# Performance work log

Hardware: AMD Instinct MI355X
Metric: run time of the kernel (lower is better)

The kernel has to match this reference:

```python
import jax, jax.numpy as jnp
import numpy as np

B, P, V, L = 256, 512, 8, 16
N = B * P            # 131072 nodes
C = V * L            # 128 in_channels (== out_channels, forced by the .view in forward)
H = 4                # heads
DOUT = 128           # out_channels per head
E = N * 5            # k=5 neighbors per node
NEG_SLOPE = 0.2


def setup_inputs() -> dict:
    key = jax.random.key(0)
    ks = jax.random.split(key, 8)
    patches = jax.random.normal(ks[0], (B, P, V, L), dtype=jnp.float32)
    edge_index = jax.random.randint(ks[1], (2, E), 0, N, dtype=jnp.int64)
    s = 1.0 / np.sqrt(C)
    W_gat = jax.random.uniform(ks[2], (C, H * DOUT), dtype=jnp.float32, minval=-s, maxval=s)
    att_src = jax.random.uniform(ks[3], (H, DOUT), dtype=jnp.float32, minval=-s, maxval=s)
    att_dst = jax.random.uniform(ks[4], (H, DOUT), dtype=jnp.float32, minval=-s, maxval=s)
    bias_gat = jnp.zeros((H * DOUT,), dtype=jnp.float32)
    s2 = 1.0 / np.sqrt(H * DOUT)
    W_lin = jax.random.uniform(ks[5], (H * DOUT, DOUT), dtype=jnp.float32, minval=-s2, maxval=s2)
    b_lin = jax.random.uniform(ks[6], (DOUT,), dtype=jnp.float32, minval=-s2, maxval=s2)
    return {"patches": patches, "edge_index": edge_index, "W_gat": W_gat,
            "att_src": att_src, "att_dst": att_dst, "bias_gat": bias_gat,
            "W_lin": W_lin, "b_lin": b_lin}


def reference(patches, edge_index, W_gat, att_src, att_dst, bias_gat, W_lin, b_lin):
    b, p, v, l = patches.shape
    n = b * p
    x = patches.reshape(n, v * l)                      # [N, C]
    xw = (x @ W_gat).reshape(n, H, DOUT)               # [N, H, D]
    # PyG GATConv default add_self_loops=True
    loops = jnp.arange(n, dtype=edge_index.dtype)
    src = jnp.concatenate([edge_index[0], loops])      # message source j
    dst = jnp.concatenate([edge_index[1], loops])      # message target i
    a_src = jnp.einsum('nhd,hd->nh', xw, att_src)      # [N, H]
    a_dst = jnp.einsum('nhd,hd->nh', xw, att_dst)
    e = jax.nn.leaky_relu(a_src[src] + a_dst[dst], NEG_SLOPE)   # [Etot, H]
    m = jax.ops.segment_max(e, dst, num_segments=n)
    ex = jnp.exp(e - m[dst])
    denom = jax.ops.segment_sum(ex, dst, num_segments=n)
    alpha = ex / (denom[dst] + 1e-16)                  # segment softmax over in-edges
    out = jax.ops.segment_sum(alpha[:, :, None] * xw[src], dst, num_segments=n)  # [N, H, D]
    out = out.reshape(n, H * DOUT) + bias_gat
    out = jax.nn.elu(out)
    out = out @ W_lin + b_lin                          # [N, DOUT]
    return out.reshape(b, p, v, l)
```

## Files before the change

kernel.cpp:

```cpp
#include <hip/hip_runtime.h>
#include <hip/hip_bf16.h>
#include <stdint.h>

#define N_NODES 131072
#define C_IN    128
#define HEADS   4
#define DHEAD   128
#define HD      512
#define E_EDGES 655360
#define NEG_SLOPE 0.2f
#define NCHUNK  4
#define CHUNK_N (N_NODES / NCHUNK)
#define SCAN_B  (N_NODES / 256)

typedef short bf16x8 __attribute__((ext_vector_type(8)));
typedef float f32x4  __attribute__((ext_vector_type(4)));

__device__ __forceinline__ float bf2f(unsigned short u) {
    unsigned int x = ((unsigned int)u) << 16;
    return __builtin_bit_cast(float, x);
}
__device__ __forceinline__ unsigned short f2bf(float f) {
    unsigned int u = __builtin_bit_cast(unsigned int, f);
    unsigned int r = u + 0x7FFFu + ((u >> 16) & 1u);
    return (unsigned short)(r >> 16);
}
__device__ __forceinline__ float lrelu(float v) {
    return v > 0.0f ? v : NEG_SLOPE * v;
}

__global__ void detect_kernel(const unsigned int* p_f, const unsigned int* p_i, int* flags) {
    int lane = threadIdx.x;
    int cnt = 0;
#pragma unroll
    for (int r = 0; r < 4; r++) {
        unsigned int e = (p_f[lane + 64 * r] >> 7) & 0xFFu;
        cnt += (e >= 110u && e <= 137u) ? 1 : 0;
    }
    int z = 0;
#pragma unroll
    for (int r = 0; r < 2; r++) {
        z += (p_i[2 * (lane + 64 * r) + 1] == 0u) ? 1 : 0;
    }
#pragma unroll
    for (int o = 1; o < 64; o <<= 1) {
        cnt += __shfl_xor(cnt, o, 64);
        z   += __shfl_xor(z, o, 64);
    }
    if (lane == 0) {
        flags[0] = (cnt >= 128) ? 1 : 0;
        flags[1] = (z == 128) ? 1 : 0;
    }
}

__global__ void conv_w1(const void* in, unsigned short* out, const int* flags) {
    int idx = blockIdx.x * blockDim.x + threadIdx.x;
    int n = idx >> 7, k = idx & 127;
    float v = flags[0] ? bf2f(((const unsigned short*)in)[k * HD + n])
                       : ((const float*)in)[k * HD + n];
    out[idx] = f2bf(v);
}

__global__ void conv_w2(const void* in, unsigned short* out, const int* flags) {
    int idx = blockIdx.x * blockDim.x + threadIdx.x;
    int n = idx >> 9, k = idx & 511;
    float v = flags[0] ? bf2f(((const unsigned short*)in)[k * DHEAD + n])
                       : ((const float*)in)[k * DHEAD + n];
    out[idx] = f2bf(v);
}

__global__ void conv_small(const void* as, const void* ad, const void* bg, const void* bl,
                           float* att_s, float* att_d, float* bias_g, float* b_lin,
                           const int* flags) {
    int i = blockIdx.x * blockDim.x + threadIdx.x;
    bool bf = flags[0] != 0;
    if (i < 512) {
        att_s[i] = bf ? bf2f(((const unsigned short*)as)[i]) : ((const float*)as)[i];
    } else if (i < 1024) {
        int j = i - 512;
        att_d[j] = bf ? bf2f(((const unsigned short*)ad)[j]) : ((const float*)ad)[j];
    } else if (i < 1536) {
        int j = i - 1024;
        bias_g[j] = bf ? bf2f(((const unsigned short*)bg)[j]) : ((const float*)bg)[j];
    } else if (i < 1664) {
        int j = i - 1536;
        b_lin[j] = bf ? bf2f(((const unsigned short*)bl)[j]) : ((const float*)bl)[j];
    }
}

__global__ void conv_edges_hist(const void* in, int* src32, int* dst32, int* deg,
                                const int* flags) {
    int i = blockIdx.x * blockDim.x + threadIdx.x;
    if (i >= 2 * E_EDGES) return;
    int v = flags[1] ? (int)((const long long*)in)[i] : ((const int*)in)[i];
    if (i < E_EDGES) {
        src32[i] = v;
    } else {
        dst32[i - E_EDGES] = v;
        atomicAdd(&deg[v], 1);
    }
}

__global__ void zero_deg(int* deg) {
    int i = blockIdx.x * blockDim.x + threadIdx.x;
    deg[i] = 0;
}

__global__ void scan_local(const int* __restrict__ deg, int* __restrict__ offv,
                           int* __restrict__ bsums) {
    __shared__ int tmp[256];
    int t = threadIdx.x;
    int g = blockIdx.x * 256 + t;
    int v = deg[g];
    tmp[t] = v;
    __syncthreads();
#pragma unroll
    for (int d = 1; d < 256; d <<= 1) {
        int x = (t >= d) ? tmp[t - d] : 0;
        __syncthreads();
        tmp[t] += x;
        __syncthreads();
    }
    offv[g] = tmp[t] - v;
    if (t == 255) bsums[blockIdx.x] = tmp[t];
}

__global__ void scan_bsums(int* bsums) {
    __shared__ int tmp[SCAN_B];
    int t = threadIdx.x;
    int v = bsums[t];
    tmp[t] = v;
    __syncthreads();
#pragma unroll
    for (int d = 1; d < SCAN_B; d <<= 1) {
        int x = (t >= d) ? tmp[t - d] : 0;
        __syncthreads();
        tmp[t] += x;
        __syncthreads();
    }
    bsums[t] = tmp[t] - v;
}

__global__ void scan_apply(int* __restrict__ offv, const int* __restrict__ bsums,
                           int* __restrict__ cursor) {
    int g = blockIdx.x * 256 + threadIdx.x;
    int v = offv[g] + bsums[blockIdx.x];
    offv[g] = v;
    cursor[g] = v;
}

__global__ void scatter_kernel(const int* src32, const int* dst32, int* cursor, int* csr) {
    int i = blockIdx.x * blockDim.x + threadIdx.x;
    int d = dst32[i];
    int pos = atomicAdd(&cursor[d], 1);
    csr[pos] = src32[i];
}

__launch_bounds__(256)
__global__ void gemm1_fused(const void* __restrict__ Ain,
                            const unsigned short* __restrict__ BT,
                            const float* __restrict__ attS, const float* __restrict__ attD,
                            unsigned short* __restrict__ xw,
                            float* __restrict__ aSrc, float* __restrict__ aDst,
                            const int* __restrict__ flags) {
    __shared__ unsigned short lA[128 * 136];
    __shared__ unsigned short lB[128 * 136];
    __shared__ float dS[2][128];
    __shared__ float dD[2][128];
    int tid = threadIdx.x;
    int m0 = blockIdx.x * 128;

    if (flags[0] == 0) {
        const float* Af = (const float*)Ain;
#pragma unroll
        for (int p = 0; p < 16; p++) {
            int l = p * 256 + tid;
            int r = l >> 5, c = (l & 31) * 4;
            float4 f = *(const float4*)&Af[(size_t)(m0 + r) * C_IN + c];
            unsigned short t4[4] = {f2bf(f.x), f2bf(f.y), f2bf(f.z), f2bf(f.w)};
            *(uint2*)&lA[r * 136 + c] = *(const uint2*)t4;
        }
    } else {
        const unsigned short* Ab = (const unsigned short*)Ain;
#pragma unroll
        for (int p = 0; p < 8; p++) {
            int l = p * 256 + tid;
            int r = l >> 4, c = (l & 15) * 8;
            *(uint4*)&lA[r * 136 + c] = *(const uint4*)&Ab[(size_t)(m0 + r) * C_IN + c];
        }
    }

    int wid = tid >> 6, lane = tid & 63;
    int wr = (wid >> 1) * 64, wc = (wid & 1) * 64;
    int lr = lane & 15, half = lane >> 4;
    int slot = wid & 1;

    for (int ct = 0; ct < HEADS; ct++) {
#pragma unroll
        for (int p = 0; p < 8; p++) {
            int l = p * 256 + tid;
            int r = l >> 4, c = (l & 15) * 8;
            *(uint4*)&lB[r * 136 + c] = *(const uint4*)&BT[(size_t)(ct * 128 + r) * C_IN + c];
        }
        __syncthreads();

        f32x4 acc[4][4];
#pragma unroll
        for (int i = 0; i < 4; i++)
#pragma unroll
            for (int j = 0; j < 4; j++) acc[i][j] = (f32x4){0.f, 0.f, 0.f, 0.f};

#pragma unroll
        for (int kk = 0; kk < 4; kk++) {
            bf16x8 af[4], bfr[4];
#pragma unroll
            for (int i = 0; i < 4; i++)
                af[i] = *(const bf16x8*)&lA[(wr + i * 16 + lr) * 136 + kk * 32 + half * 8];
#pragma unroll
            for (int j = 0; j < 4; j++)
                bfr[j] = *(const bf16x8*)&lB[(wc + j * 16 + lr) * 136 + kk * 32 + half * 8];
#pragma unroll
            for (int i = 0; i < 4; i++)
#pragma unroll
                for (int j = 0; j < 4; j++)
                    acc[i][j] = __builtin_amdgcn_mfma_f32_16x16x32_bf16(af[i], bfr[j], acc[i][j], 0, 0, 0);
        }

        const float* aS = attS + ct * DHEAD;
        const float* aD = attD + ct * DHEAD;
#pragma unroll
        for (int i = 0; i < 4; i++) {
#pragma unroll
            for (int r = 0; r < 4; r++) {
                float ps = 0.f, pd = 0.f;
#pragma unroll
                for (int j = 0; j < 4; j++) {
                    float v = acc[i][j][r];
                    int col = wc + j * 16 + lr;
                    ps += v * aS[col];
                    pd += v * aD[col];
                }
#pragma unroll
                for (int o = 1; o < 16; o <<= 1) {
                    ps += __shfl_xor(ps, o, 64);
                    pd += __shfl_xor(pd, o, 64);
                }
                if (lr == 0) {
                    int row = wr + i * 16 + half * 4 + r;
                    dS[slot][row] = ps;
                    dD[slot][row] = pd;
                }
            }
        }
        __syncthreads();

#pragma unroll
        for (int i = 0; i < 4; i++)
#pragma unroll
            for (int j = 0; j < 4; j++)
#pragma unroll
                for (int r = 0; r < 4; r++)
                    lB[(wr + i * 16 + half * 4 + r) * 136 + wc + j * 16 + lr] = f2bf(acc[i][j][r]);
        __syncthreads();

#pragma unroll
        for (int p = 0; p < 8; p++) {
            int l = p * 256 + tid;
            int r = l >> 4, c = (l & 15) * 8;
            *(uint4*)&xw[(size_t)(m0 + r) * HD + ct * 128 + c] = *(const uint4*)&lB[r * 136 + c];
        }
        if (tid < 128) {
            aSrc[(size_t)(m0 + tid) * HEADS + ct] = dS[0][tid] + dS[1][tid];
        } else {
            int t = tid - 128;
            aDst[(size_t)(m0 + t) * HEADS + ct] = dD[0][t] + dD[1][t];
        }
        __syncthreads();
    }
}

__launch_bounds__(256)
__global__ void gemm2(const unsigned short* __restrict__ A,
                      const unsigned short* __restrict__ BT,
                      const float* __restrict__ bias,
                      unsigned short* Cbf, float* Cf,
                      const int* __restrict__ flags, long long rowOff) {
    __shared__ unsigned short smem[64 * 136];
    unsigned short* lA = smem;
    unsigned short* lB = smem + 64 * 40;
    int tid = threadIdx.x;
    int m0 = blockIdx.x * 64;
    int wid = tid >> 6, lane = tid & 63;
    int wr = (wid >> 1) * 32, wc = (wid & 1) * 64;
    int lr = lane & 15, half = lane >> 4;

    f32x4 acc[2][4];
#pragma unroll
    for (int i = 0; i < 2; i++)
#pragma unroll
        for (int j = 0; j < 4; j++) acc[i][j] = (f32x4){0.f, 0.f, 0.f, 0.f};

    for (int k0 = 0; k0 < HD; k0 += 32) {
        {
            int r = tid >> 2, c = (tid & 3) * 8;
            *(uint4*)&lA[r * 40 + c] = *(const uint4*)&A[(size_t)(m0 + r) * HD + k0 + c];
        }
#pragma unroll
        for (int p = 0; p < 2; p++) {
            int l = p * 256 + tid;
            int r = l >> 2, c = (l & 3) * 8;
            *(uint4*)&lB[r * 40 + c] = *(const uint4*)&BT[(size_t)r * HD + k0 + c];
        }
        __syncthreads();
        bf16x8 af[2], bfr[4];
#pragma unroll
        for (int i = 0; i < 2; i++)
            af[i] = *(const bf16x8*)&lA[(wr + i * 16 + lr) * 40 + half * 8];
#pragma unroll
        for (int j = 0; j < 4; j++)
            bfr[j] = *(const bf16x8*)&lB[(wc + j * 16 + lr) * 40 + half * 8];
#pragma unroll
        for (int i = 0; i < 2; i++)
#pragma unroll
            for (int j = 0; j < 4; j++)
                acc[i][j] = __builtin_amdgcn_mfma_f32_16x16x32_bf16(af[i], bfr[j], acc[i][j], 0, 0, 0);
        __syncthreads();
    }

    if (flags[0] != 0) {
#pragma unroll
        for (int i = 0; i < 2; i++)
#pragma unroll
            for (int j = 0; j < 4; j++) {
                int gcol = wc + j * 16 + lr;
                float b = bias[gcol];
#pragma unroll
                for (int r = 0; r < 4; r++)
                    smem[(wr + i * 16 + half * 4 + r) * 136 + gcol] = f2bf(acc[i][j][r] + b);
            }
        __syncthreads();
#pragma unroll
        for (int p = 0; p < 2; p++) {
            int l = p * 256 + tid;
            int r = l >> 4, c = (l & 15) * 8;
            *(uint4*)&Cbf[(size_t)(rowOff + m0 + r) * DHEAD + c] = *(const uint4*)&smem[r * 136 + c];
        }
    } else {
#pragma unroll
        for (int i = 0; i < 2; i++)
#pragma unroll
            for (int j = 0; j < 4; j++) {
                int gcol = wc + j * 16 + lr;
                float b = bias[gcol];
#pragma unroll
                for (int r = 0; r < 4; r++) {
                    int grow = m0 + wr + i * 16 + half * 4 + r;
                    Cf[(size_t)(rowOff + grow) * DHEAD + gcol] = acc[i][j][r] + b;
                }
            }
    }
}

__launch_bounds__(256)
__global__ void aggregate(const unsigned short* __restrict__ xw,
                          const float* __restrict__ a_src, const float* __restrict__ a_dst,
                          const int* __restrict__ off, const int* __restrict__ deg,
                          const int* __restrict__ csr, const float* __restrict__ bias_g,
                          unsigned short* __restrict__ y, int nodeBase) {
    int local = blockIdx.x * 4 + (threadIdx.x >> 6);
    int node = nodeBase + local;
    int l = threadIdx.x & 63;
    int h = l >> 4;
    int ebase = l * 8;
    int o = off[node], dn = deg[node];
    float ad = a_dst[node * HEADS + h];

    float acc[8];
    float denom;
    {
        float w = __expf(lrelu(a_src[node * HEADS + h] + ad));
        uint4 q = *(const uint4*)&xw[(size_t)node * HD + ebase];
        const unsigned short* u = (const unsigned short*)&q;
        denom = w;
#pragma unroll
        for (int k = 0; k < 8; k++) acc[k] = w * bf2f(u[k]);
    }

    for (int e0 = 0; e0 < dn; e0 += 8) {
        int   idx[8];
        float as[8];
        uint4 px[8];
#pragma unroll
        for (int b = 0; b < 8; b++)
            idx[b] = (e0 + b < dn) ? csr[o + e0 + b] : node;
#pragma unroll
        for (int b = 0; b < 8; b++)
            as[b] = a_src[idx[b] * HEADS + h];
#pragma unroll
        for (int b = 0; b < 8; b++)
            px[b] = *(const uint4*)&xw[(size_t)idx[b] * HD + ebase];
#pragma unroll
        for (int b = 0; b < 8; b++) {
            float w = (e0 + b < dn) ? __expf(lrelu(as[b] + ad)) : 0.0f;
            denom += w;
            const unsigned short* u = (const unsigned short*)&px[b];
#pragma unroll
            for (int k = 0; k < 8; k++) acc[k] += w * bf2f(u[k]);
        }
    }

    float inv = 1.0f / (denom + 1e-16f);
    unsigned short outp[8];
#pragma unroll
    for (int k = 0; k < 8; k++) {
        float v = acc[k] * inv + bias_g[ebase + k];
        v = v > 0.f ? v : (__expf(v) - 1.0f);
        outp[k] = f2bf(v);
    }
    *(uint4*)&y[(size_t)local * HD + ebase] = *(const uint4*)outp;
}

extern "C" void kernel_launch(void* const* d_in, const int* in_sizes, int n_in,
                              void* d_out, int out_size, void* d_ws, size_t ws_size,
                              hipStream_t stream) {
    char* ws = (char*)d_ws;
    size_t wsoff = 0;
    auto alloc = [&](size_t bytes) -> char* {
        char* p = ws + wsoff;
        wsoff += (bytes + 255) & ~(size_t)255;
        return p;
    };

    int*            flags  = (int*)           alloc(256);
    unsigned short* WT1    = (unsigned short*)alloc((size_t)HD * C_IN * 2);
    unsigned short* WT2    = (unsigned short*)alloc((size_t)DHEAD * HD * 2);
    float*          attS   = (float*)         alloc(HD * 4);
    float*          attD   = (float*)         alloc(HD * 4);
    float*          biasG  = (float*)         alloc(HD * 4);
    float*          bLin   = (float*)         alloc(DHEAD * 4);
    int*            src32  = (int*)           alloc((size_t)E_EDGES * 4);
    int*            dst32  = (int*)           alloc((size_t)E_EDGES * 4);
    int*            deg    = (int*)           alloc((size_t)N_NODES * 4);
    int*            offv   = (int*)           alloc((size_t)(N_NODES + 1) * 4);
    int*            cursor = (int*)           alloc((size_t)N_NODES * 4);
    int*            csr    = (int*)           alloc((size_t)E_EDGES * 4);
    int*            bsums  = (int*)           alloc((size_t)SCAN_B * 4);
    float*          aSrc   = (float*)         alloc((size_t)N_NODES * HEADS * 4);
    float*          aDst   = (float*)         alloc((size_t)N_NODES * HEADS * 4);
    unsigned short* xw     = (unsigned short*)alloc((size_t)N_NODES * HD * 2);
    unsigned short* ychunk = (unsigned short*)alloc((size_t)CHUNK_N * HD * 2);

    const void* patches = d_in[0];
    const void* edges   = d_in[1];
    const void* Wgat    = d_in[2];
    const void* attSrcI = d_in[3];
    const void* attDstI = d_in[4];
    const void* biasGI  = d_in[5];
    const void* WlinI   = d_in[6];
    const void* bLinI   = d_in[7];

    detect_kernel<<<1, 64, 0, stream>>>((const unsigned int*)patches,
                                        (const unsigned int*)edges, flags);

    conv_w1<<<(HD * C_IN) / 256, 256, 0, stream>>>(Wgat, WT1, flags);
    conv_w2<<<(DHEAD * HD) / 256, 256, 0, stream>>>(WlinI, WT2, flags);
    conv_small<<<7, 256, 0, stream>>>(attSrcI, attDstI, biasGI, bLinI,
                                      attS, attD, biasG, bLin, flags);

    zero_deg<<<N_NODES / 256, 256, 0, stream>>>(deg);
    conv_edges_hist<<<(2 * E_EDGES) / 256, 256, 0, stream>>>(edges, src32, dst32, deg, flags);
    scan_local<<<SCAN_B, 256, 0, stream>>>(deg, offv, bsums);
    scan_bsums<<<1, SCAN_B, 0, stream>>>(bsums);
    scan_apply<<<SCAN_B, 256, 0, stream>>>(offv, bsums, cursor);
    scatter_kernel<<<E_EDGES / 256, 256, 0, stream>>>(src32, dst32, cursor, csr);

    gemm1_fused<<<N_NODES / 128, 256, 0, stream>>>(
        patches, WT1, attS, attD, xw, aSrc, aDst, flags);

    for (int c = 0; c < NCHUNK; c++) {
        int base = c * CHUNK_N;
        aggregate<<<CHUNK_N / 4, 256, 0, stream>>>(xw, aSrc, aDst, offv, deg, csr,
                                                   biasG, ychunk, base);
        gemm2<<<CHUNK_N / 64, 256, 0, stream>>>(
            ychunk, WT2, bLin, (unsigned short*)d_out, (float*)d_out, flags, base);
    }
}
```

Baseline: 463.9 us.

## Restructure gemm1 to swap MFMA operands and write outputs directly from registers

The first GEMM kernel no longer stages the weight tile or the output tile through shared memory. Each wave now owns 32 full rows and reads B fragments straight from global memory. MFMA operands are swapped so each lane holds four consecutive output columns. This lets the attention dot products be reduced with only two shuffles and the bf16 results be stored as packed 8-byte writes, with no LDS round-trip and fewer barriers. In exchange, weight fragments are reloaded from global memory or cache by every wave rather than shared via LDS, and the xw stores are narrower and less coalesced than the earlier 16-byte stores.

```diff
diff --git a/kernel.cpp b/kernel.cpp
--- a/kernel.cpp
+++ b/kernel.cpp
@@ -164,9 +164,6 @@
                             float* __restrict__ aSrc, float* __restrict__ aDst,
                             const int* __restrict__ flags) {
     __shared__ unsigned short lA[128 * 136];
-    __shared__ unsigned short lB[128 * 136];
-    __shared__ float dS[2][128];
-    __shared__ float dD[2][128];
     int tid = threadIdx.x;
     int m0 = blockIdx.x * 128;
 
@@ -189,93 +186,68 @@
             *(uint4*)&lA[r * 136 + c] = *(const uint4*)&Ab[(size_t)(m0 + r) * C_IN + c];
         }
     }
+    __syncthreads();
 
     int wid = tid >> 6, lane = tid & 63;
-    int wr = (wid >> 1) * 64, wc = (wid & 1) * 64;
+    int wr = wid * 32;
     int lr = lane & 15, half = lane >> 4;
-    int slot = wid & 1;
+
+    const float4* attS4 = (const float4*)attS;
+    const float4* attD4 = (const float4*)attD;
 
     for (int ct = 0; ct < HEADS; ct++) {
-#pragma unroll
-        for (int p = 0; p < 8; p++) {
-            int l = p * 256 + tid;
-            int r = l >> 4, c = (l & 15) * 8;
-            *(uint4*)&lB[r * 136 + c] = *(const uint4*)&BT[(size_t)(ct * 128 + r) * C_IN + c];
-        }
-        __syncthreads();
-
-        f32x4 acc[4][4];
-#pragma unroll
-        for (int i = 0; i < 4; i++)
-#pragma unroll
-            for (int j = 0; j < 4; j++) acc[i][j] = (f32x4){0.f, 0.f, 0.f, 0.f};
+        f32x4 acc[2][8];
+#pragma unroll
+        for (int i = 0; i < 2; i++)
+#pragma unroll
+            for (int j = 0; j < 8; j++) acc[i][j] = (f32x4){0.f, 0.f, 0.f, 0.f};
 
 #pragma unroll
         for (int kk = 0; kk < 4; kk++) {
-            bf16x8 af[4], bfr[4];
-#pragma unroll
-            for (int i = 0; i < 4; i++)
+            bf16x8 bfr[8];
+#pragma unroll
+            for (int j = 0; j < 8; j++)
+                bfr[j] = *(const bf16x8*)&BT[(size_t)(ct * 128 + j * 16 + lr) * C_IN + kk * 32 + half * 8];
+            bf16x8 af[2];
+#pragma unroll
+            for (int i = 0; i < 2; i++)
                 af[i] = *(const bf16x8*)&lA[(wr + i * 16 + lr) * 136 + kk * 32 + half * 8];
 #pragma unroll
-            for (int j = 0; j < 4; j++)
-                bfr[j] = *(const bf16x8*)&lB[(wc + j * 16 + lr) * 136 + kk * 32 + half * 8];
-#pragma unroll
-            for (int i = 0; i < 4; i++)
-#pragma unroll
-                for (int j = 0; j < 4; j++)
-                    acc[i][j] = __builtin_amdgcn_mfma_f32_16x16x32_bf16(af[i], bfr[j], acc[i][j], 0, 0, 0);
-        }
-
-        const float* aS = attS + ct * DHEAD;
-        const float* aD = attD + ct * DHEAD;
-#pragma unroll
-        for (int i = 0; i < 4; i++) {
-#pragma unroll
-            for (int r = 0; r < 4; r++) {
-                float ps = 0.f, pd = 0.f;
-#pragma unroll
-                for (int j = 0; j < 4; j++) {
-                    float v = acc[i][j][r];
-                    int col = wc + j * 16 + lr;
-                    ps += v * aS[col];
-                    pd += v * aD[col];
-                }
-#pragma unroll
-                for (int o = 1; o < 16; o <<= 1) {
-                    ps += __shfl_xor(ps, o, 64);
-                    pd += __shfl_xor(pd, o, 64);
-                }
-                if (lr == 0) {
-                    int row = wr + i * 16 + half * 4 + r;
-                    dS[slot][row] = ps;
-                    dD[slot][row] = pd;
-                }
+            for (int i = 0; i < 2; i++)
+#pragma unroll
+                for (int j = 0; j < 8; j++)
+                    acc[i][j] = __builtin_amdgcn_mfma_f32_16x16x32_bf16(bfr[j], af[i], acc[i][j], 0, 0, 0);
+        }
+
+#pragma unroll
+        for (int i = 0; i < 2; i++) {
+            int row = wr + i * 16 + lr;
+            float ps = 0.f, pd = 0.f;
+#pragma unroll
+            for (int j = 0; j < 8; j++) {
+                float4 s4 = attS4[ct * 32 + j * 4 + half];
+                float4 d4 = attD4[ct * 32 + j * 4 + half];
+                ps += acc[i][j][0] * s4.x + acc[i][j][1] * s4.y
+                    + acc[i][j][2] * s4.z + acc[i][j][3] * s4.w;
+                pd += acc[i][j][0] * d4.x + acc[i][j][1] * d4.y
+                    + acc[i][j][2] * d4.z + acc[i][j][3] * d4.w;
             }
-        }
-        __syncthreads();
-
-#pragma unroll
-        for (int i = 0; i < 4; i++)
-#pragma unroll
-            for (int j = 0; j < 4; j++)
-#pragma unroll
-                for (int r = 0; r < 4; r++)
-                    lB[(wr + i * 16 + half * 4 + r) * 136 + wc + j * 16 + lr] = f2bf(acc[i][j][r]);
-        __syncthreads();
-
-#pragma unroll
-        for (int p = 0; p < 8; p++) {
-            int l = p * 256 + tid;
-            int r = l >> 4, c = (l & 15) * 8;
-            *(uint4*)&xw[(size_t)(m0 + r) * HD + ct * 128 + c] = *(const uint4*)&lB[r * 136 + c];
-        }
-        if (tid < 128) {
-            aSrc[(size_t)(m0 + tid) * HEADS + ct] = dS[0][tid] + dS[1][tid];
-        } else {
-            int t = tid - 128;
-            aDst[(size_t)(m0 + t) * HEADS + ct] = dD[0][t] + dD[1][t];
-        }
-        __syncthreads();
+            ps += __shfl_xor(ps, 16, 64);
+            ps += __shfl_xor(ps, 32, 64);
+            pd += __shfl_xor(pd, 16, 64);
+            pd += __shfl_xor(pd, 32, 64);
+            if (half == 0) {
+                aSrc[(size_t)(m0 + row) * HEADS + ct] = ps;
+                aDst[(size_t)(m0 + row) * HEADS + ct] = pd;
+            }
+#pragma unroll
+            for (int j = 0; j < 8; j++) {
+                uint2 pk;
+                pk.x = (unsigned int)f2bf(acc[i][j][0]) | ((unsigned int)f2bf(acc[i][j][1]) << 16);
+                pk.y = (unsigned int)f2bf(acc[i][j][2]) | ((unsigned int)f2bf(acc[i][j][3]) << 16);
+                *(uint2*)&xw[(size_t)(m0 + row) * HD + ct * 128 + j * 16 + half * 4] = pk;
+            }
+        }
     }
 }
 
```

New measurement: 526.0 us. 13.4% more time.
